# Kernel optimization log

Hardware: AMD Instinct MI355X
Metric: run time of the kernel (lower is better)

Reference implementation:

```python
import jax, jax.numpy as jnp
import numpy as np

B = 16          # number of point clouds in the batch
N_COARSE = 1024 # coarse points per cloud
N_FINE = 4096   # fine (skip) points per cloud
C_IN = 256
C_SKIP = 128
K = 3
EPS = 1e-16


def setup_inputs() -> dict:
    key = jax.random.key(0)
    ks = jax.random.split(key, 8)
    x = jax.random.normal(ks[0], (B * N_COARSE, C_IN), dtype=jnp.float32)
    pos = jax.random.uniform(ks[1], (B * N_COARSE, 3), dtype=jnp.float32)
    x_skip = jax.random.normal(ks[2], (B * N_FINE, C_SKIP), dtype=jnp.float32)
    pos_skip = jax.random.uniform(ks[3], (B * N_FINE, 3), dtype=jnp.float32)
    batch = jnp.repeat(jnp.arange(B, dtype=jnp.int64), N_COARSE)
    batch_skip = jnp.repeat(jnp.arange(B, dtype=jnp.int64), N_FINE)
    W1 = jax.random.normal(ks[4], (C_IN + C_SKIP, 256), dtype=jnp.float32) * (1.0 / np.sqrt(C_IN + C_SKIP))
    b1 = jnp.zeros((256,), dtype=jnp.float32)
    W2 = jax.random.normal(ks[5], (256, 256), dtype=jnp.float32) * (1.0 / np.sqrt(256))
    b2 = jnp.zeros((256,), dtype=jnp.float32)
    return {"x": x, "pos": pos, "batch": batch, "x_skip": x_skip,
            "pos_skip": pos_skip, "batch_skip": batch_skip,
            "W1": W1, "b1": b1, "W2": W2, "b2": b2}


def _knn_interpolate(x, pos, pos_skip):
    # Equal-sized clouds: reshape to [B, N, *] and do batched kNN.
    xc = x.reshape(B, N_COARSE, C_IN)
    pc = pos.reshape(B, N_COARSE, 3)
    pf = pos_skip.reshape(B, N_FINE, 3)
    # squared pairwise distances [B, M, N]
    d2 = (jnp.sum(pf * pf, -1)[:, :, None]
          + jnp.sum(pc * pc, -1)[:, None, :]
          - 2.0 * jnp.einsum('bmd,bnd->bmn', pf, pc))
    d2 = jnp.maximum(d2, 0.0)
    neg_d2k, idx = jax.lax.top_k(-d2, K)          # k smallest distances
    w = 1.0 / jnp.maximum(-neg_d2k, EPS)          # [B, M, K] inverse-sq-dist weights
    gathered = jax.vmap(lambda f, i: f[i])(xc, idx)  # [B, M, K, C]
    y = jnp.sum(w[..., None] * gathered, axis=2) / jnp.sum(w, axis=2, keepdims=True)
    return y.reshape(B * N_FINE, C_IN)


def reference(x, pos, batch, x_skip, pos_skip, batch_skip, W1, b1, W2, b2):
    x_interp = _knn_interpolate(x, pos, pos_skip)          # [B*M, C_IN]
    h = jnp.concatenate([x_interp, x_skip], axis=1)        # [B*M, C_IN + C_SKIP]
    h = jax.nn.relu(h @ W1 + b1)
    out = jax.nn.relu(h @ W2 + b2)
    return out
```

## Files before the change

### kernel.cpp

```cpp
#include <hip/hip_runtime.h>

typedef float  f32x4  __attribute__((ext_vector_type(4)));
typedef short  short8 __attribute__((ext_vector_type(8)));
typedef unsigned short ushort_t;
typedef ushort_t us4   __attribute__((ext_vector_type(4)));

#define NCOARSE 1024
#define NFINE   4096

__device__ __forceinline__ ushort_t f2bf(float f){
  union { float f; unsigned u; } a; a.f = f;
  unsigned u = a.u;
  return (ushort_t)((u + 0x7fffu + ((u >> 16) & 1u)) >> 16);
}

__device__ __forceinline__ f32x4 splat4(float v){ f32x4 t = {v, v, v, v}; return t; }

__global__ void prep_w(const float* __restrict__ W, ushort_t* __restrict__ Wp, int nelem){
  int e = blockIdx.x * 256 + threadIdx.x;
  if (e >= nelem) return;
  int j    = e & 7;
  int lane = (e >> 3) & 63;
  int g    = e >> 9;
  int nb   = g & 15;
  int kc   = g >> 4;
  int k = kc * 32 + (lane >> 4) * 8 + j;
  int n = nb * 16 + (lane & 15);
  Wp[e] = f2bf(W[k * 256 + n]);
}

__global__ __launch_bounds__(256) void knn_kernel(const float* __restrict__ pos,
                           const float* __restrict__ pos_skip,
                           int* __restrict__ knn_i, float* __restrict__ knn_w){
  __shared__ f32x4 cand[8][129];
  const int tid = threadIdx.x;
  const int b   = blockIdx.x >> 7;
  const int m   = blockIdx.x * 32 + (tid >> 3);
  const int chunk = tid & 7;

  const float* p = pos + (size_t)b * NCOARSE * 3;
  for (int c = tid; c < NCOARSE; c += 256){
    float x = p[3*c], y = p[3*c+1], z = p[3*c+2];
    float sc = __fadd_rn(__fadd_rn(__fmul_rn(x,x), __fmul_rn(y,y)), __fmul_rn(z,z));
    f32x4 v = { x, y, z, sc };
    cand[c >> 7][c & 127] = v;
  }
  __syncthreads();

  const float* q = pos_skip + (size_t)m * 3;
  float qx = q[0], qy = q[1], qz = q[2];
  float sf = __fadd_rn(__fadd_rn(__fmul_rn(qx,qx), __fmul_rn(qy,qy)), __fmul_rn(qz,qz));

  float d0 = 1e30f, d1 = 1e30f, d2 = 1e30f;
  int   i0 = 0,     i1 = 0,     i2 = 0;
  const int gbase = chunk * 128;
  #pragma unroll 4
  for (int i = 0; i < 128; ++i){
    f32x4 v = cand[chunk][i];
    float dot = __fadd_rn(__fadd_rn(__fmul_rn(qx, v.x), __fmul_rn(qy, v.y)),
                          __fmul_rn(qz, v.z));
    float d = __fsub_rn(__fadd_rn(sf, v.w), __fmul_rn(2.0f, dot));
    d = fmaxf(d, 0.0f);
    if (d < d2){
      int gi = gbase + i;
      if (d < d1){
        d2 = d1; i2 = i1;
        if (d < d0){ d1 = d0; i1 = i0; d0 = d; i0 = gi; }
        else       { d1 = d;  i1 = gi; }
      } else { d2 = d; i2 = gi; }
    }
  }

  #pragma unroll
  for (int mlev = 1; mlev <= 4; mlev <<= 1){
    float e0 = __shfl_xor(d0, mlev), e1 = __shfl_xor(d1, mlev), e2 = __shfl_xor(d2, mlev);
    int   j0 = __shfl_xor(i0, mlev), j1 = __shfl_xor(i1, mlev), j2 = __shfl_xor(i2, mlev);
    #pragma unroll
    for (int s = 0; s < 3; ++s){
      float e = (s == 0) ? e0 : (s == 1) ? e1 : e2;
      int   j = (s == 0) ? j0 : (s == 1) ? j1 : j2;
      bool l2 = (e < d2) || (e == d2 && j < i2);
      if (l2){
        bool l1 = (e < d1) || (e == d1 && j < i1);
        if (l1){
          d2 = d1; i2 = i1;
          bool l0 = (e < d0) || (e == d0 && j < i0);
          if (l0){ d1 = d0; i1 = i0; d0 = e; i0 = j; }
          else   { d1 = e;  i1 = j; }
        } else { d2 = e; i2 = j; }
      }
    }
  }

  if (chunk == 0){
    float w0 = 1.0f / fmaxf(d0, 1e-16f);
    float w1 = 1.0f / fmaxf(d1, 1e-16f);
    float w2 = 1.0f / fmaxf(d2, 1e-16f);
    float ws = __fadd_rn(__fadd_rn(w0, w1), w2);
    knn_i[3*m]   = b * NCOARSE + i0;
    knn_i[3*m+1] = b * NCOARSE + i1;
    knn_i[3*m+2] = b * NCOARSE + i2;
    knn_w[3*m]   = w0 / ws;
    knn_w[3*m+1] = w1 / ws;
    knn_w[3*m+2] = w2 / ws;
  }
}

__global__ __launch_bounds__(256, 3)
void fused_fp(const float* __restrict__ x, const float* __restrict__ x_skip,
              const int* __restrict__ knn_i, const float* __restrict__ knn_w,
              const ushort_t* __restrict__ W1p, const float* __restrict__ b1,
              const ushort_t* __restrict__ W2p, const float* __restrict__ b2,
              float* __restrict__ out){
  __shared__ ushort_t hbuf[64 * 384];
  char* h1b = (char*)hbuf;
  char* h2b = (char*)hbuf;
  const int tid  = threadIdx.x;
  const int lb   = ((blockIdx.x & 7) << 7) + (blockIdx.x >> 3);
  const int row0 = lb * 64;

  {
    const int r   = tid >> 2;
    const int sub = tid & 3;
    const int m   = row0 + r;

    const f32x4* xsr = (const f32x4*)(x_skip + (size_t)m * 128);
    f32x4 xs[8];
    #pragma unroll
    for (int it = 0; it < 8; ++it) xs[it] = xsr[it * 4 + sub];

    int i0 = knn_i[3*m], i1 = knn_i[3*m+1], i2 = knn_i[3*m+2];
    float w0 = knn_w[3*m], w1 = knn_w[3*m+1], w2 = knn_w[3*m+2];
    const f32x4* x0 = (const f32x4*)(x + (size_t)i0 * 256);
    const f32x4* x1 = (const f32x4*)(x + (size_t)i1 * 256);
    const f32x4* x2 = (const f32x4*)(x + (size_t)i2 * 256);

    #pragma unroll
    for (int it = 0; it < 16; ++it){
      int c4 = it * 4 + sub;
      f32x4 v = x0[c4] * w0 + x1[c4] * w1 + x2[c4] * w2;
      int byte = (r * 768 + c4 * 8) ^ ((r & 7) << 4);
      us4 pk = { f2bf(v.x), f2bf(v.y), f2bf(v.z), f2bf(v.w) };
      *(us4*)(h1b + byte) = pk;
    }
    #pragma unroll
    for (int it = 0; it < 8; ++it){
      int c4 = it * 4 + sub;
      f32x4 v = xs[it];
      int byte = (r * 768 + 512 + c4 * 8) ^ ((r & 7) << 4);
      us4 pk = { f2bf(v.x), f2bf(v.y), f2bf(v.z), f2bf(v.w) };
      *(us4*)(h1b + byte) = pk;
    }
  }
  __syncthreads();

  const int wp  = tid >> 6;
  const int lane = tid & 63;
  const int lhi = lane >> 4;
  const int llo = lane & 15;

  f32x4 acc[4][4];
  #pragma unroll
  for (int nbp = 0; nbp < 4; ++nbp){
    float bb = b1[wp * 64 + nbp * 16 + llo];
    #pragma unroll
    for (int mb = 0; mb < 4; ++mb) acc[mb][nbp] = splat4(bb);
  }
  #pragma unroll
  for (int kk = 0; kk < 12; ++kk){
    short8 af[4];
    #pragma unroll
    for (int mb = 0; mb < 4; ++mb){
      int r = mb * 16 + llo;
      int byte = (r * 768 + kk * 64 + lhi * 16) ^ ((r & 7) << 4);
      af[mb] = *(const short8*)(h1b + byte);
    }
    short8 bfr[4];
    #pragma unroll
    for (int nbp = 0; nbp < 4; ++nbp)
      bfr[nbp] = *(const short8*)(W1p + ((size_t)((kk * 16 + wp * 4 + nbp) * 64 + lane)) * 8);
    #pragma unroll
    for (int mb = 0; mb < 4; ++mb)
      #pragma unroll
      for (int nbp = 0; nbp < 4; ++nbp)
        acc[mb][nbp] = __builtin_amdgcn_mfma_f32_16x16x32_bf16(af[mb], bfr[nbp], acc[mb][nbp], 0, 0, 0);
  }
  __syncthreads();

  #pragma unroll
  for (int mb = 0; mb < 4; ++mb)
    #pragma unroll
    for (int nbp = 0; nbp < 4; ++nbp)
      #pragma unroll
      for (int rg = 0; rg < 4; ++rg){
        int r   = mb * 16 + lhi * 4 + rg;
        int col = wp * 64 + nbp * 16 + llo;
        int byte = (r * 512 + col * 2) ^ ((r & 7) << 4);
        *(ushort_t*)(h2b + byte) = f2bf(fmaxf(acc[mb][nbp][rg], 0.0f));
      }
  __syncthreads();

  f32x4 acc2[4][4];
  #pragma unroll
  for (int nbp = 0; nbp < 4; ++nbp){
    float bb = b2[wp * 64 + nbp * 16 + llo];
    #pragma unroll
    for (int mb = 0; mb < 4; ++mb) acc2[mb][nbp] = splat4(bb);
  }
  #pragma unroll
  for (int kk = 0; kk < 8; ++kk){
    short8 af[4];
    #pragma unroll
    for (int mb = 0; mb < 4; ++mb){
      int r = mb * 16 + llo;
      int byte = (r * 512 + kk * 64 + lhi * 16) ^ ((r & 7) << 4);
      af[mb] = *(const short8*)(h2b + byte);
    }
    short8 bfr[4];
    #pragma unroll
    for (int nbp = 0; nbp < 4; ++nbp)
      bfr[nbp] = *(const short8*)(W2p + ((size_t)((kk * 16 + wp * 4 + nbp) * 64 + lane)) * 8);
    #pragma unroll
    for (int mb = 0; mb < 4; ++mb)
      #pragma unroll
      for (int nbp = 0; nbp < 4; ++nbp)
        acc2[mb][nbp] = __builtin_amdgcn_mfma_f32_16x16x32_bf16(af[mb], bfr[nbp], acc2[mb][nbp], 0, 0, 0);
  }
  #pragma unroll
  for (int mb = 0; mb < 4; ++mb)
    #pragma unroll
    for (int nbp = 0; nbp < 4; ++nbp)
      #pragma unroll
      for (int rg = 0; rg < 4; ++rg){
        int row = row0 + mb * 16 + lhi * 4 + rg;
        int col = wp * 64 + nbp * 16 + llo;
        out[(size_t)row * 256 + col] = fmaxf(acc2[mb][nbp][rg], 0.0f);
      }
}

extern "C" void kernel_launch(void* const* d_in, const int* in_sizes, int n_in,
                              void* d_out, int out_size, void* d_ws, size_t ws_size,
                              hipStream_t stream){
  (void)in_sizes; (void)n_in; (void)out_size; (void)ws_size;
  const float* x        = (const float*)d_in[0];
  const float* pos      = (const float*)d_in[1];
  const float* x_skip   = (const float*)d_in[3];
  const float* pos_skip = (const float*)d_in[4];
  const float* W1 = (const float*)d_in[6];
  const float* b1 = (const float*)d_in[7];
  const float* W2 = (const float*)d_in[8];
  const float* b2 = (const float*)d_in[9];
  float* out = (float*)d_out;
  char* ws = (char*)d_ws;
  ushort_t* W1p = (ushort_t*)(ws);
  ushort_t* W2p = (ushort_t*)(ws + 196608);
  int*      ki  = (int*)(ws + 327680);
  float*    kw  = (float*)(ws + 1114112);

  hipLaunchKernelGGL(prep_w, dim3(384), dim3(256), 0, stream, W1, W1p, 98304);
  hipLaunchKernelGGL(prep_w, dim3(256), dim3(256), 0, stream, W2, W2p, 65536);
  hipLaunchKernelGGL(knn_kernel, dim3(2048), dim3(256), 0, stream, pos, pos_skip, ki, kw);
  hipLaunchKernelGGL(fused_fp, dim3(1024), dim3(256), 0, stream,
                     x, x_skip, ki, kw, W1p, b1, W2p, b2, out);
}
```

Measured before the change: 88.03 us.

## Split gather/interpolation into separate kernel staging bf16 h1 in global memory

Adds a stage_h1 kernel that does the kNN gather, weighted interpolation, and concat with x_skip, writing a bf16 [rows,384] buffer to workspace. A new gemm_fp kernel then loads that buffer with coalesced vector loads into swizzled LDS and runs both MLP layers. The intent is to separate the latency-bound scattered gather from the MFMA GEMM so each kernel can keep a higher occupancy. In exchange it adds an extra kernel launch and a round trip of the intermediate buffer through global memory. It falls back to the old fused kernel when the workspace is too small.

```diff
diff --git a/kernel.cpp b/kernel.cpp
--- a/kernel.cpp
+++ b/kernel.cpp
@@ -4,6 +4,7 @@
 typedef short  short8 __attribute__((ext_vector_type(8)));
 typedef unsigned short ushort_t;
 typedef ushort_t us4   __attribute__((ext_vector_type(4)));
+typedef ushort_t us8   __attribute__((ext_vector_type(8)));
 
 #define NCOARSE 1024
 #define NFINE   4096
@@ -106,6 +107,159 @@
   }
 }
 
+__global__ __launch_bounds__(256, 4)
+void stage_h1(const float* __restrict__ x, const float* __restrict__ x_skip,
+              const int* __restrict__ knn_i, const float* __restrict__ knn_w,
+              ushort_t* __restrict__ h1g){
+  const int tid = threadIdx.x;
+  const int lb  = ((blockIdx.x & 7) << 8) + (blockIdx.x >> 3);
+  const int r   = tid >> 3;
+  const int sub = tid & 7;
+  const int m   = lb * 32 + r;
+
+  int i0 = knn_i[3*m], i1 = knn_i[3*m+1], i2 = knn_i[3*m+2];
+  float w0 = knn_w[3*m], w1 = knn_w[3*m+1], w2 = knn_w[3*m+2];
+  const f32x4* x0 = (const f32x4*)(x + (size_t)i0 * 256);
+  const f32x4* x1 = (const f32x4*)(x + (size_t)i1 * 256);
+  const f32x4* x2 = (const f32x4*)(x + (size_t)i2 * 256);
+  ushort_t* hrow = h1g + (size_t)m * 384;
+
+  #pragma unroll
+  for (int k = 0; k < 4; ++k){
+    int c8 = k * 8 + sub;
+    f32x4 a0 = x0[c8*2], a1 = x0[c8*2+1];
+    f32x4 b0 = x1[c8*2], b1 = x1[c8*2+1];
+    f32x4 c0 = x2[c8*2], c1 = x2[c8*2+1];
+    f32x4 vl = a0 * w0 + b0 * w1 + c0 * w2;
+    f32x4 vh = a1 * w0 + b1 * w1 + c1 * w2;
+    us8 pk = { f2bf(vl.x), f2bf(vl.y), f2bf(vl.z), f2bf(vl.w),
+               f2bf(vh.x), f2bf(vh.y), f2bf(vh.z), f2bf(vh.w) };
+    *(us8*)(hrow + c8 * 8) = pk;
+  }
+  const f32x4* xs = (const f32x4*)(x_skip + (size_t)m * 128);
+  #pragma unroll
+  for (int k = 0; k < 2; ++k){
+    int c8 = k * 8 + sub;
+    f32x4 a0 = xs[c8*2], a1 = xs[c8*2+1];
+    us8 pk = { f2bf(a0.x), f2bf(a0.y), f2bf(a0.z), f2bf(a0.w),
+               f2bf(a1.x), f2bf(a1.y), f2bf(a1.z), f2bf(a1.w) };
+    *(us8*)(hrow + 256 + c8 * 8) = pk;
+  }
+}
+
+__global__ __launch_bounds__(256, 3)
+void gemm_fp(const ushort_t* __restrict__ h1g,
+             const ushort_t* __restrict__ W1p, const float* __restrict__ b1,
+             const ushort_t* __restrict__ W2p, const float* __restrict__ b2,
+             float* __restrict__ out){
+  __shared__ ushort_t hbuf[64 * 384];
+  char* h1b = (char*)hbuf;
+  char* h2b = (char*)hbuf;
+  const int tid  = threadIdx.x;
+  const int lb   = ((blockIdx.x & 7) << 7) + (blockIdx.x >> 3);
+  const int row0 = lb * 64;
+
+  {
+    const char* src = (const char*)h1g + (size_t)row0 * 768;
+    short8 st[12];
+    #pragma unroll
+    for (int it = 0; it < 12; ++it){
+      int gb = it * 4096 + tid * 16;
+      st[it] = *(const short8*)(src + gb);
+    }
+    #pragma unroll
+    for (int it = 0; it < 12; ++it){
+      int gb  = it * 4096 + tid * 16;
+      int row = gb / 768;
+      *(short8*)(h1b + (gb ^ ((row & 7) << 4))) = st[it];
+    }
+  }
+  __syncthreads();
+
+  const int wp  = tid >> 6;
+  const int lane = tid & 63;
+  const int lhi = lane >> 4;
+  const int llo = lane & 15;
+
+  f32x4 acc[4][4];
+  #pragma unroll
+  for (int nbp = 0; nbp < 4; ++nbp){
+    float bb = b1[wp * 64 + nbp * 16 + llo];
+    #pragma unroll
+    for (int mb = 0; mb < 4; ++mb) acc[mb][nbp] = splat4(bb);
+  }
+  #pragma unroll
+  for (int kk = 0; kk < 12; ++kk){
+    short8 af[4];
+    #pragma unroll
+    for (int mb = 0; mb < 4; ++mb){
+      int r = mb * 16 + llo;
+      int byte = (r * 768 + kk * 64 + lhi * 16) ^ ((r & 7) << 4);
+      af[mb] = *(const short8*)(h1b + byte);
+    }
+    short8 bfr[4];
+    #pragma unroll
+    for (int nbp = 0; nbp < 4; ++nbp)
+      bfr[nbp] = *(const short8*)(W1p + ((size_t)((kk * 16 + wp * 4 + nbp) * 64 + lane)) * 8);
+    #pragma unroll
+    for (int mb = 0; mb < 4; ++mb)
+      #pragma unroll
+      for (int nbp = 0; nbp < 4; ++nbp)
+        acc[mb][nbp] = __builtin_amdgcn_mfma_f32_16x16x32_bf16(af[mb], bfr[nbp], acc[mb][nbp], 0, 0, 0);
+  }
+  __syncthreads();
+
+  #pragma unroll
+  for (int mb = 0; mb < 4; ++mb)
+    #pragma unroll
+    for (int nbp = 0; nbp < 4; ++nbp)
+      #pragma unroll
+      for (int rg = 0; rg < 4; ++rg){
+        int r   = mb * 16 + lhi * 4 + rg;
+        int col = wp * 64 + nbp * 16 + llo;
+        int byte = (r * 512 + col * 2) ^ ((r & 7) << 4);
+        *(ushort_t*)(h2b + byte) = f2bf(fmaxf(acc[mb][nbp][rg], 0.0f));
+      }
+  __syncthreads();
+
+  f32x4 acc2[4][4];
+  #pragma unroll
+  for (int nbp = 0; nbp < 4; ++nbp){
+    float bb = b2[wp * 64 + nbp * 16 + llo];
+    #pragma unroll
+    for (int mb = 0; mb < 4; ++mb) acc2[mb][nbp] = splat4(bb);
+  }
+  #pragma unroll
+  for (int kk = 0; kk < 8; ++kk){
+    short8 af[4];
+    #pragma unroll
+    for (int mb = 0; mb < 4; ++mb){
+      int r = mb * 16 + llo;
+      int byte = (r * 512 + kk * 64 + lhi * 16) ^ ((r & 7) << 4);
+      af[mb] = *(const short8*)(h2b + byte);
+    }
+    short8 bfr[4];
+    #pragma unroll
+    for (int nbp = 0; nbp < 4; ++nbp)
+      bfr[nbp] = *(const short8*)(W2p + ((size_t)((kk * 16 + wp * 4 + nbp) * 64 + lane)) * 8);
+    #pragma unroll
+    for (int mb = 0; mb < 4; ++mb)
+      #pragma unroll
+      for (int nbp = 0; nbp < 4; ++nbp)
+        acc2[mb][nbp] = __builtin_amdgcn_mfma_f32_16x16x32_bf16(af[mb], bfr[nbp], acc2[mb][nbp], 0, 0, 0);
+  }
+  #pragma unroll
+  for (int mb = 0; mb < 4; ++mb)
+    #pragma unroll
+    for (int nbp = 0; nbp < 4; ++nbp)
+      #pragma unroll
+      for (int rg = 0; rg < 4; ++rg){
+        int row = row0 + mb * 16 + lhi * 4 + rg;
+        int col = wp * 64 + nbp * 16 + llo;
+        out[(size_t)row * 256 + col] = fmaxf(acc2[mb][nbp][rg], 0.0f);
+      }
+}
+
 __global__ __launch_bounds__(256, 3)
 void fused_fp(const float* __restrict__ x, const float* __restrict__ x_skip,
               const int* __restrict__ knn_i, const float* __restrict__ knn_w,
@@ -118,23 +272,19 @@
   const int tid  = threadIdx.x;
   const int lb   = ((blockIdx.x & 7) << 7) + (blockIdx.x >> 3);
   const int row0 = lb * 64;
-
   {
     const int r   = tid >> 2;
     const int sub = tid & 3;
     const int m   = row0 + r;
-
     const f32x4* xsr = (const f32x4*)(x_skip + (size_t)m * 128);
     f32x4 xs[8];
     #pragma unroll
     for (int it = 0; it < 8; ++it) xs[it] = xsr[it * 4 + sub];
-
     int i0 = knn_i[3*m], i1 = knn_i[3*m+1], i2 = knn_i[3*m+2];
     float w0 = knn_w[3*m], w1 = knn_w[3*m+1], w2 = knn_w[3*m+2];
     const f32x4* x0 = (const f32x4*)(x + (size_t)i0 * 256);
     const f32x4* x1 = (const f32x4*)(x + (size_t)i1 * 256);
     const f32x4* x2 = (const f32x4*)(x + (size_t)i2 * 256);
-
     #pragma unroll
     for (int it = 0; it < 16; ++it){
       int c4 = it * 4 + sub;
@@ -153,12 +303,10 @@
     }
   }
   __syncthreads();
-
   const int wp  = tid >> 6;
   const int lane = tid & 63;
   const int lhi = lane >> 4;
   const int llo = lane & 15;
-
   f32x4 acc[4][4];
   #pragma unroll
   for (int nbp = 0; nbp < 4; ++nbp){
@@ -186,7 +334,6 @@
         acc[mb][nbp] = __builtin_amdgcn_mfma_f32_16x16x32_bf16(af[mb], bfr[nbp], acc[mb][nbp], 0, 0, 0);
   }
   __syncthreads();
-
   #pragma unroll
   for (int mb = 0; mb < 4; ++mb)
     #pragma unroll
@@ -199,7 +346,6 @@
         *(ushort_t*)(h2b + byte) = f2bf(fmaxf(acc[mb][nbp][rg], 0.0f));
       }
   __syncthreads();
-
   f32x4 acc2[4][4];
   #pragma unroll
   for (int nbp = 0; nbp < 4; ++nbp){
@@ -241,7 +387,7 @@
 extern "C" void kernel_launch(void* const* d_in, const int* in_sizes, int n_in,
                               void* d_out, int out_size, void* d_ws, size_t ws_size,
                               hipStream_t stream){
-  (void)in_sizes; (void)n_in; (void)out_size; (void)ws_size;
+  (void)in_sizes; (void)n_in; (void)out_size;
   const float* x        = (const float*)d_in[0];
   const float* pos      = (const float*)d_in[1];
   const float* x_skip   = (const float*)d_in[3];
@@ -256,10 +402,19 @@
   ushort_t* W2p = (ushort_t*)(ws + 196608);
   int*      ki  = (int*)(ws + 327680);
   float*    kw  = (float*)(ws + 1114112);
+  ushort_t* h1g = (ushort_t*)(ws + 1900544);
+  const size_t WS_NEED = 1900544ull + 50331648ull;
 
   hipLaunchKernelGGL(prep_w, dim3(384), dim3(256), 0, stream, W1, W1p, 98304);
   hipLaunchKernelGGL(prep_w, dim3(256), dim3(256), 0, stream, W2, W2p, 65536);
   hipLaunchKernelGGL(knn_kernel, dim3(2048), dim3(256), 0, stream, pos, pos_skip, ki, kw);
-  hipLaunchKernelGGL(fused_fp, dim3(1024), dim3(256), 0, stream,
-                     x, x_skip, ki, kw, W1p, b1, W2p, b2, out);
-}
+  if (ws_size >= WS_NEED){
+    hipLaunchKernelGGL(stage_h1, dim3(2048), dim3(256), 0, stream,
+                       x, x_skip, ki, kw, h1g);
+    hipLaunchKernelGGL(gemm_fp, dim3(1024), dim3(256), 0, stream,
+                       h1g, W1p, b1, W2p, b2, out);
+  } else {
+    hipLaunchKernelGGL(fused_fp, dim3(1024), dim3(256), 0, stream,
+                       x, x_skip, ki, kw, W1p, b1, W2p, b2, out);
+  }
+}
```

After: 109.2 us. 1.24x slower.

## Double-buffer weight fragments through LDS with register prefetch in fused MLP

Applied to the files above, without the earlier changes.

Weight fragments for both GEMMs are now prefetched one k-step ahead into registers and staged through a double-buffered LDS area. Each k-step reads the B operand from LDS instead of global memory. The aim is to hide the global load latency of the weights behind the MFMA work. In exchange it adds a block-wide barrier per k-step and 32KB more LDS, and launch bounds drop from 3 to 2 blocks per CU. Each wave only reads back its own slice, so the LDS round trip gives no sharing between waves.

```diff
diff --git a/kernel.cpp b/kernel.cpp
--- a/kernel.cpp
+++ b/kernel.cpp
@@ -106,35 +106,68 @@
   }
 }
 
-__global__ __launch_bounds__(256, 3)
+#define LDW(DST, WP, F)                                                     \
+  { _Pragma("unroll")                                                       \
+    for (int i_ = 0; i_ < 4; ++i_)                                          \
+      DST[i_] = *(const short8*)((WP) + ((size_t)(((F) + i_) * 64 + lane)) * 8); }
+
+#define STW(BUF, SRC)                                                       \
+  { _Pragma("unroll")                                                       \
+    for (int i_ = 0; i_ < 4; ++i_)                                          \
+      *(short8*)&wbuf[BUF][(wp * 4 + i_) * 512 + lane * 8] = SRC[i_]; }
+
+#define KSTEP(LDSBASE, STR, KK, BUF, ACC)                                   \
+  { short8 af_[4], bf_[4];                                                  \
+    _Pragma("unroll")                                                       \
+    for (int mb_ = 0; mb_ < 4; ++mb_){                                      \
+      int r_ = mb_ * 16 + llo;                                              \
+      int byte_ = (r_ * (STR) + (KK) * 64 + lhi * 16) ^ ((r_ & 7) << 4);    \
+      af_[mb_] = *(const short8*)((LDSBASE) + byte_);                       \
+    }                                                                       \
+    _Pragma("unroll")                                                       \
+    for (int nb_ = 0; nb_ < 4; ++nb_)                                       \
+      bf_[nb_] = *(const short8*)&wbuf[BUF][(wp * 4 + nb_) * 512 + lane * 8];\
+    _Pragma("unroll")                                                       \
+    for (int mb_ = 0; mb_ < 4; ++mb_)                                       \
+      _Pragma("unroll")                                                     \
+      for (int nb_ = 0; nb_ < 4; ++nb_)                                     \
+        ACC[mb_][nb_] = __builtin_amdgcn_mfma_f32_16x16x32_bf16(            \
+            af_[mb_], bf_[nb_], ACC[mb_][nb_], 0, 0, 0); }
+
+__global__ __launch_bounds__(256, 2)
 void fused_fp(const float* __restrict__ x, const float* __restrict__ x_skip,
               const int* __restrict__ knn_i, const float* __restrict__ knn_w,
               const ushort_t* __restrict__ W1p, const float* __restrict__ b1,
               const ushort_t* __restrict__ W2p, const float* __restrict__ b2,
               float* __restrict__ out){
   __shared__ ushort_t hbuf[64 * 384];
+  __shared__ ushort_t wbuf[2][8192];
   char* h1b = (char*)hbuf;
   char* h2b = (char*)hbuf;
   const int tid  = threadIdx.x;
   const int lb   = ((blockIdx.x & 7) << 7) + (blockIdx.x >> 3);
   const int row0 = lb * 64;
+  const int wp   = tid >> 6;
+  const int lane = tid & 63;
+  const int lhi  = lane >> 4;
+  const int llo  = lane & 15;
+
+  short8 wst[4];
+  LDW(wst, W1p, 0 * 16 + wp * 4);
 
   {
     const int r   = tid >> 2;
     const int sub = tid & 3;
     const int m   = row0 + r;
-
     const f32x4* xsr = (const f32x4*)(x_skip + (size_t)m * 128);
     f32x4 xs[8];
     #pragma unroll
     for (int it = 0; it < 8; ++it) xs[it] = xsr[it * 4 + sub];
-
     int i0 = knn_i[3*m], i1 = knn_i[3*m+1], i2 = knn_i[3*m+2];
     float w0 = knn_w[3*m], w1 = knn_w[3*m+1], w2 = knn_w[3*m+2];
     const f32x4* x0 = (const f32x4*)(x + (size_t)i0 * 256);
     const f32x4* x1 = (const f32x4*)(x + (size_t)i1 * 256);
     const f32x4* x2 = (const f32x4*)(x + (size_t)i2 * 256);
-
     #pragma unroll
     for (int it = 0; it < 16; ++it){
       int c4 = it * 4 + sub;
@@ -152,12 +185,9 @@
       *(us4*)(h1b + byte) = pk;
     }
   }
+  STW(0, wst);
+  LDW(wst, W1p, 1 * 16 + wp * 4);
   __syncthreads();
-
-  const int wp  = tid >> 6;
-  const int lane = tid & 63;
-  const int lhi = lane >> 4;
-  const int llo = lane & 15;
 
   f32x4 acc[4][4];
   #pragma unroll
@@ -168,24 +198,13 @@
   }
   #pragma unroll
   for (int kk = 0; kk < 12; ++kk){
-    short8 af[4];
-    #pragma unroll
-    for (int mb = 0; mb < 4; ++mb){
-      int r = mb * 16 + llo;
-      int byte = (r * 768 + kk * 64 + lhi * 16) ^ ((r & 7) << 4);
-      af[mb] = *(const short8*)(h1b + byte);
-    }
-    short8 bfr[4];
-    #pragma unroll
-    for (int nbp = 0; nbp < 4; ++nbp)
-      bfr[nbp] = *(const short8*)(W1p + ((size_t)((kk * 16 + wp * 4 + nbp) * 64 + lane)) * 8);
-    #pragma unroll
-    for (int mb = 0; mb < 4; ++mb)
-      #pragma unroll
-      for (int nbp = 0; nbp < 4; ++nbp)
-        acc[mb][nbp] = __builtin_amdgcn_mfma_f32_16x16x32_bf16(af[mb], bfr[nbp], acc[mb][nbp], 0, 0, 0);
-  }
-  __syncthreads();
+    STW((kk + 1) & 1, wst);
+    if (kk < 10)      { LDW(wst, W1p, (kk + 2) * 16 + wp * 4); }
+    else if (kk == 10){ LDW(wst, W2p, 0 * 16 + wp * 4); }
+    else              { LDW(wst, W2p, 1 * 16 + wp * 4); }
+    KSTEP(h1b, 768, kk, kk & 1, acc);
+    __syncthreads();
+  }
 
   #pragma unroll
   for (int mb = 0; mb < 4; ++mb)
@@ -208,24 +227,13 @@
     for (int mb = 0; mb < 4; ++mb) acc2[mb][nbp] = splat4(bb);
   }
   #pragma unroll
-  for (int kk = 0; kk < 8; ++kk){
-    short8 af[4];
-    #pragma unroll
-    for (int mb = 0; mb < 4; ++mb){
-      int r = mb * 16 + llo;
-      int byte = (r * 512 + kk * 64 + lhi * 16) ^ ((r & 7) << 4);
-      af[mb] = *(const short8*)(h2b + byte);
-    }
-    short8 bfr[4];
-    #pragma unroll
-    for (int nbp = 0; nbp < 4; ++nbp)
-      bfr[nbp] = *(const short8*)(W2p + ((size_t)((kk * 16 + wp * 4 + nbp) * 64 + lane)) * 8);
-    #pragma unroll
-    for (int mb = 0; mb < 4; ++mb)
-      #pragma unroll
-      for (int nbp = 0; nbp < 4; ++nbp)
-        acc2[mb][nbp] = __builtin_amdgcn_mfma_f32_16x16x32_bf16(af[mb], bfr[nbp], acc2[mb][nbp], 0, 0, 0);
-  }
+  for (int t = 0; t < 8; ++t){
+    if (t < 7) STW((t + 1) & 1, wst);
+    if (t < 6) { LDW(wst, W2p, (t + 2) * 16 + wp * 4); }
+    KSTEP(h2b, 512, t, t & 1, acc2);
+    if (t < 7) __syncthreads();
+  }
+
   #pragma unroll
   for (int mb = 0; mb < 4; ++mb)
     #pragma unroll
```

Result: no change. 89.72 us (+1.9%).
